# Optimization experiments

Measured on AMD Instinct MI355X. Metric: run time of the kernel, lower is better.

## Reference

```python
import jax, jax.numpy as jnp
import numpy as np

DIM = 512
NUM_ITEM = 2048
K = 10


def setup_inputs() -> dict:
    key = jax.random.key(0)
    k1, k2, k3 = jax.random.split(key, 3)
    input1 = jax.random.normal(k1, (16, DIM, 32, 32), dtype=jnp.float32)
    input2 = jax.random.normal(k2, (16, DIM, 32, 32), dtype=jnp.float32)
    stdv = 1.0 / np.sqrt(DIM)
    mempool = jax.random.uniform(k3, (NUM_ITEM, DIM), minval=-stdv, maxval=stdv, dtype=jnp.float32)
    return {"input1": input1, "input2": input2, "mempool": mempool}


def _memorize(x, mempool):
    # x: [B, C, H, W] with C == DIM
    B, C, H, W = x.shape
    q = jnp.transpose(x, (0, 2, 3, 1)).reshape(-1, C)      # [N, C]
    att = jax.nn.softmax(q @ mempool.T, axis=1)            # [N, num_item]
    val, idx = jax.lax.top_k(att, K)                       # [N, K]
    val = jax.nn.softmax(val, axis=1)                      # renormalize top-k
    # scatter(val into zeros) @ mempool == gather rows of mempool and combine
    out = jnp.einsum('nk,nkd->nd', val, mempool[idx])      # [N, C]
    return jnp.transpose(out.reshape(B, H, W, C), (0, 3, 1, 2))


def reference(input1, input2, mempool):
    return (_memorize(input1, mempool), _memorize(input2, mempool))
```

## Files before the change

### kernel.cpp

```cpp
#include <hip/hip_runtime.h>
#include <math.h>

typedef __attribute__((ext_vector_type(4))) float f4;
typedef __attribute__((ext_vector_type(8))) _Float16 f16x8;
typedef __attribute__((ext_vector_type(8))) short bf16x8;
typedef __attribute__((ext_vector_type(4))) unsigned short u16x4;
typedef unsigned int u32;
typedef unsigned short u16;

#define DIMC  512
#define NITEM 2048
#define TK    10
#define WSP   (NITEM * DIMC)

#define TPB    512
#define PXB    64
#define RIT    256
#define NRND   8
#define NSLICE 16

#define QB_SZ  12288
#define Q_PL   4096
#define SSTR   66
#define LDS_BYTES 67584
#define MV_F 0
#define MI_F 5120
#define MM_F 10240
#define MS_F 10752
#define WB_F 11264
#define IB_F 11904

#define KSWZ(i) (((i) ^ ((i) >> 2)) & 3)

union h16 { _Float16 h; u16 u; };

__device__ __forceinline__ u32 bf16_rne(float f) {
    u32 u = __float_as_uint(f);
    return (u + 0x7fffu + ((u >> 16) & 1u)) >> 16;
}

__device__ __forceinline__ void split3(float f, u16& ph, u16& pb, u16& pr) {
    h16 a; a.h = (_Float16)f;
    float f0 = (float)a.h;
    ph = a.u;
    pb = (u16)bf16_rne(f);
    pr = (u16)bf16_rne(f - f0);
}

__global__ __launch_bounds__(256)
void preconv_kernel(const float* __restrict__ mp, u16* __restrict__ ws)
{
    int idx = (blockIdx.x * 256 + threadIdx.x) * 4;
    int i  = idx >> 9;
    int k0 = idx & 511;
    f4 v = *(const f4*)(mp + (size_t)i * 512 + k0);
    int s  = k0 >> 5, kl = k0 & 31;
    int lh = (kl >> 2) & 3, pair = kl >> 4;
    u16x4 pH, pB, pR;
#pragma unroll
    for (int e = 0; e < 4; ++e) {
        u16 h, b, r; split3(v[e], h, b, r);
        pH[e] = h; pB[e] = b; pR[e] = r;
    }
    size_t base = (size_t)(i >> 4) * 8192 + (size_t)s * 512
                + (size_t)(lh * 16 + (i & 15)) * 8 + pair * 4;
    *(u16x4*)(ws + 0 * WSP + base) = pH;
    *(u16x4*)(ws + 1 * WSP + base) = pB;
    *(u16x4*)(ws + 2 * WSP + base) = pR;
}

__global__ __launch_bounds__(TPB, 4)
void memorize_mfma(const float* __restrict__ x0, const float* __restrict__ x1,
                   const float* __restrict__ mp, const u16* __restrict__ ws,
                   float* __restrict__ out)
{
    extern __shared__ char ldsb[];
    float* ldsf = (float*)ldsb;

    const int t    = threadIdx.x;
    const int lane = t & 63;
    const int w    = t >> 6;
    const int blk  = blockIdx.x;
    const int img  = blk >> 4;
    const int n0   = (blk & 15) * PXB;
    const int b    = img & 15;

    const float* x  = (img < 16) ? x0 : x1;
    const float* xb = x + (size_t)b * (DIMC * 1024);
    float* ob = out + (img < 16 ? (size_t)0 : (size_t)16 * DIMC * 1024)
                    + (size_t)b * (DIMC * 1024);

    const int l15 = lane & 15;
    const int lh  = lane >> 4;
    const int ksw = lh ^ KSWZ(l15);
    const int ig  = w >> 1;
    const int pg  = w & 1;

    const int qp = t & 63;
    const int g  = t >> 6;

    float tv[TK]; int tix[TK];
#pragma unroll
    for (int q = 0; q < TK; ++q) { tv[q] = -INFINITY; tix[q] = 0x7fffffff; }
    float rm = -INFINITY, rs = 0.0f;

    const int scl  = t & 31;
    const int spx  = (t >> 5) << 2;
    const int spos = (((scl >> 2) & 3) << 3) + ((scl >> 4) << 2) + (scl & 3);
    const int sslot = spos >> 3;
    const int soff  = (spos & 7) << 1;

    const u16* aw = ws + (size_t)lane * 8 + (size_t)(ig * 4) * 8192;

    const int qfb = (pg << 11) + (l15 << 6) + (ksw << 4);

#define STAGE_Q(S, BUF)                                                        \
    {                                                                          \
        const float* src = xb + (size_t)(((S) << 5) + scl) * 1024 + n0 + spx;  \
        f4 v = *(const f4*)src;                                                \
        _Pragma("unroll")                                                      \
        for (int e = 0; e < 4; ++e) {                                          \
            int px = spx + e;                                                  \
            u16 h, bb, rr; split3(v[e], h, bb, rr);                            \
            int ro = (BUF) * QB_SZ + (px << 6)                                 \
                   + (((sslot ^ KSWZ(px)) << 4) | soff);                       \
            *(u16*)(ldsb + ro)            = h;                                 \
            *(u16*)(ldsb + ro + Q_PL)     = bb;                                \
            *(u16*)(ldsb + ro + 2 * Q_PL) = rr;                                \
        }                                                                      \
    }

#define ALOAD(IT, S)                                                           \
    {                                                                          \
        const u16* ap = ar + ((size_t)(IT) << 13) + ((S) << 9);                \
        aH[IT] = *(const f16x8*) (ap + 0 * WSP);                               \
        aB[IT] = *(const bf16x8*)(ap + 1 * WSP);                               \
        aR[IT] = *(const bf16x8*)(ap + 2 * WSP);                               \
    }

#pragma unroll 1
    for (int r = 0; r < NRND; ++r) {
        const u16* ar = aw + ((size_t)r << 17);
        f4 acc[4][2];
#pragma unroll
        for (int it = 0; it < 4; ++it)
#pragma unroll
            for (int pt = 0; pt < 2; ++pt) acc[it][pt] = (f4){0.f, 0.f, 0.f, 0.f};

        __syncthreads();
        STAGE_Q(0, 0)
        __syncthreads();

#pragma unroll 1
        for (int s = 0; s < NSLICE; ++s) {
            const int cur = s & 1;

            f16x8 aH[4]; bf16x8 aB[4], aR[4];
            ALOAD(0, s)
            ALOAD(1, s)

            if (s + 1 < NSLICE) STAGE_Q(s + 1, cur ^ 1)

            const char* qc = ldsb + cur * QB_SZ + qfb;
            f16x8 qH[2]; bf16x8 qB[2], qR[2];
#pragma unroll
            for (int pt = 0; pt < 2; ++pt) {
                qH[pt] = *(const f16x8*) (qc + 0 * Q_PL + pt * 1024);
                qB[pt] = *(const bf16x8*)(qc + 1 * Q_PL + pt * 1024);
                qR[pt] = *(const bf16x8*)(qc + 2 * Q_PL + pt * 1024);
            }

#pragma unroll
            for (int it = 0; it < 4; ++it) {
                if (it < 2) ALOAD(it + 2, s)
#pragma unroll
                for (int pt = 0; pt < 2; ++pt) {
                    f4 c = acc[it][pt];
                    c = __builtin_amdgcn_mfma_f32_16x16x32_f16 (aH[it], qH[pt], c, 0, 0, 0);
                    c = __builtin_amdgcn_mfma_f32_16x16x32_bf16(aB[it], qR[pt], c, 0, 0, 0);
                    c = __builtin_amdgcn_mfma_f32_16x16x32_bf16(aR[it], qB[pt], c, 0, 0, 0);
                    acc[it][pt] = c;
                }
            }
            __syncthreads();
        }

#pragma unroll
        for (int it = 0; it < 4; ++it) {
#pragma unroll
            for (int pt = 0; pt < 2; ++pt) {
                int row = (ig << 6) + (it << 4) + (lh << 2);
                int col = (pg << 5) + (pt << 4) + l15;
                float* sp = ldsf + row * SSTR + col;
                sp[0 * SSTR] = acc[it][pt][0];
                sp[1 * SSTR] = acc[it][pt][1];
                sp[2 * SSTR] = acc[it][pt][2];
                sp[3 * SSTR] = acc[it][pt][3];
            }
        }
        __syncthreads();

        float mloc = rm;
#pragma unroll 4
        for (int jj = 0; jj < 32; ++jj) {
            int   il = (g << 5) + jj;
            float v  = ldsf[il * SSTR + qp];
            mloc = fmaxf(mloc, v);
            if (v > tv[TK - 1]) {
                int   id = r * RIT + il;
                float cv = v; int ci = id;
#pragma unroll
                for (int q = 0; q < TK; ++q) {
                    bool  gt = cv > tv[q];
                    float nv = gt ? tv[q]  : cv;
                    int   ni = gt ? tix[q] : ci;
                    tv[q]  = gt ? cv : tv[q];
                    tix[q] = gt ? ci : tix[q];
                    cv = nv; ci = ni;
                }
            }
        }
        rs *= __expf(rm - mloc);
        rm = mloc;
#pragma unroll 4
        for (int jj = 0; jj < 32; ++jj) {
            int   il = (g << 5) + jj;
            float v  = ldsf[il * SSTR + qp];
            rs += __expf(v - rm);
        }
    }

    __syncthreads();
    {
#pragma unroll
        for (int q = 0; q < TK; ++q) {
            ldsf[MV_F + (qp * 8 + g) * TK + q] = tv[q];
            ldsf[MI_F + (qp * 8 + g) * TK + q] = __int_as_float(tix[q]);
        }
        ldsf[MM_F + qp * 8 + g] = rm;
        ldsf[MS_F + qp * 8 + g] = rs;
    }
    __syncthreads();

    if (t < 64) {
        const int p = t;
        float gm[8], gs[8];
#pragma unroll
        for (int G = 0; G < 8; ++G) {
            gm[G] = ldsf[MM_F + p * 8 + G];
            gs[G] = ldsf[MS_F + p * 8 + G];
        }
        float mstar = gm[0];
#pragma unroll
        for (int G = 1; G < 8; ++G) mstar = fmaxf(mstar, gm[G]);
        float Z = 0.0f;
#pragma unroll
        for (int G = 0; G < 8; ++G) Z += gs[G] * __expf(gm[G] - mstar);

        int h0=0,h1=0,h2=0,h3=0,h4=0,h5=0,h6=0,h7=0;
        float ov[TK]; int oi[TK];
#pragma unroll
        for (int o = 0; o < TK; ++o) {
            float bv = -INFINITY; int bi = 0x7fffffff; int bg = 0;
#define SEL(G, HG)                                                               \
            {                                                                    \
                float v  = ldsf[MV_F + (p * 8 + G) * TK + (HG)];                 \
                int   id = __float_as_int(ldsf[MI_F + (p * 8 + G) * TK + (HG)]); \
                if (v > bv || (v == bv && id < bi)) { bv = v; bi = id; bg = G; } \
            }
            SEL(0, h0) SEL(1, h1) SEL(2, h2) SEL(3, h3)
            SEL(4, h4) SEL(5, h5) SEL(6, h6) SEL(7, h7)
#undef SEL
            ov[o] = bv; oi[o] = bi;
            h0 += (bg == 0); h1 += (bg == 1); h2 += (bg == 2); h3 += (bg == 3);
            h4 += (bg == 4); h5 += (bg == 5); h6 += (bg == 6); h7 += (bg == 7);
        }
        float pv[TK];
#pragma unroll
        for (int o = 0; o < TK; ++o) pv[o] = __expf(ov[o] - mstar) / Z;
        float pmax = pv[0];
        float wgt[TK]; float W = 0.0f;
#pragma unroll
        for (int o = 0; o < TK; ++o) { wgt[o] = __expf(pv[o] - pmax); W += wgt[o]; }
#pragma unroll
        for (int o = 0; o < TK; ++o) {
            ldsf[WB_F + p * TK + o] = wgt[o] / W;
            ldsf[IB_F + p * TK + o] = __int_as_float(oi[o]);
        }
    }
    __syncthreads();

    {
        const int ep = t & 63, cg = t >> 6;
        float wr[TK]; const float* rows[TK];
#pragma unroll
        for (int o = 0; o < TK; ++o) {
            wr[o]   = ldsf[WB_F + ep * TK + o];
            rows[o] = mp + (size_t)__float_as_int(ldsf[IB_F + ep * TK + o]) * DIMC;
        }
        float* obase = ob + n0 + ep;
#pragma unroll 4
        for (int cc = 0; cc < 16; ++cc) {
            int c = cg * 64 + cc * 4;
            f4 a = {0.0f, 0.0f, 0.0f, 0.0f};
#pragma unroll
            for (int o = 0; o < TK; ++o) {
                f4 rv = *(const f4*)(rows[o] + c);
#pragma unroll
                for (int z = 0; z < 4; ++z) a[z] = fmaf(wr[o], rv[z], a[z]);
            }
#pragma unroll
            for (int z = 0; z < 4; ++z) obase[(size_t)(c + z) * 1024] = a[z];
        }
    }
#undef STAGE_Q
#undef ALOAD
}

extern "C" void kernel_launch(void* const* d_in, const int* in_sizes, int n_in,
                              void* d_out, int out_size, void* d_ws, size_t ws_size,
                              hipStream_t stream) {
    const float* x0  = (const float*)d_in[0];
    const float* x1  = (const float*)d_in[1];
    const float* mpl = (const float*)d_in[2];
    float* out = (float*)d_out;
    u16* ws = (u16*)d_ws;

    preconv_kernel<<<dim3(1024), dim3(256), 0, stream>>>(mpl, ws);
    memorize_mfma<<<dim3(512), dim3(TPB), LDS_BYTES, stream>>>(x0, x1, mpl, ws, out);
}
```

Measured before the change: 579.5 us.

## Pre-split inputs into MFMA fragment layout in workspace, load directly from global

Adds a preconversion kernel that splits both inputs into fp16/bf16/residual planes laid out in MFMA fragment order inside the workspace. The main kernel then reads the query fragments straight from global memory instead of staging them through double-buffered LDS, which removes the per-slice barriers and the in-loop conversion. This costs an extra pass that writes about 200MB of workspace and reads it back, and depends on the workspace being large enough; otherwise the old LDS-staged path is used.

```diff
diff --git a/kernel.cpp b/kernel.cpp
--- a/kernel.cpp
+++ b/kernel.cpp
@@ -12,6 +12,8 @@
 #define NITEM 2048
 #define TK    10
 #define WSP   (NITEM * DIMC)
+#define XWSP  (32 * DIMC * 1024)
+#define QWS_OFF (3 * WSP)
 
 #define TPB    512
 #define PXB    64
@@ -19,10 +21,7 @@
 #define NRND   8
 #define NSLICE 16
 
-#define QB_SZ  12288
-#define Q_PL   4096
 #define SSTR   66
-#define LDS_BYTES 67584
 #define MV_F 0
 #define MI_F 5120
 #define MM_F 10240
@@ -30,6 +29,9 @@
 #define WB_F 11264
 #define IB_F 11904
 
+#define QB_SZ  12288
+#define Q_PL   4096
+#define LDS_BYTES 67584
 #define KSWZ(i) (((i) ^ ((i) >> 2)) & 3)
 
 union h16 { _Float16 h; u16 u; };
@@ -69,10 +71,244 @@
     *(u16x4*)(ws + 2 * WSP + base) = pR;
 }
 
+__global__ __launch_bounds__(256)
+void preconv_x_kernel(const float* __restrict__ x0, const float* __restrict__ x1,
+                      u16* __restrict__ ws)
+{
+    int T   = blockIdx.x * 256 + threadIdx.x;
+    int px  = T & 1023;
+    int c4  = (T >> 10) & 127;
+    int img = T >> 17;
+    const float* x = (img < 16) ? x0 : x1;
+    const float* src = x + ((size_t)(img & 15) * 512 + (size_t)c4 * 4) * 1024 + px;
+    int s = c4 >> 3, pair = (c4 >> 2) & 1, lh = c4 & 3;
+    u16x4 pH, pB, pR;
+#pragma unroll
+    for (int j = 0; j < 4; ++j) {
+        u16 h, b, r; split3(src[(size_t)j * 1024], h, b, r);
+        pH[j] = h; pB[j] = b; pR[j] = r;
+    }
+    size_t base = (size_t)QWS_OFF
+                + (size_t)(img * 64 + (px >> 4)) * 8192 + (size_t)s * 512
+                + (size_t)((lh * 16 + (px & 15)) << 3) + pair * 4;
+    *(u16x4*)(ws + base + 0 * (size_t)XWSP) = pH;
+    *(u16x4*)(ws + base + 1 * (size_t)XWSP) = pB;
+    *(u16x4*)(ws + base + 2 * (size_t)XWSP) = pR;
+}
+
 __global__ __launch_bounds__(TPB, 4)
-void memorize_mfma(const float* __restrict__ x0, const float* __restrict__ x1,
-                   const float* __restrict__ mp, const u16* __restrict__ ws,
-                   float* __restrict__ out)
+void memorize_direct(const float* __restrict__ mp, const u16* __restrict__ ws,
+                     float* __restrict__ out)
+{
+    __shared__ float ldsf[16896];
+
+    const int t    = threadIdx.x;
+    const int lane = t & 63;
+    const int w    = t >> 6;
+    const int blk  = blockIdx.x;
+    const int img  = blk >> 4;
+    const int n0   = (blk & 15) * PXB;
+
+    float* ob = out + (img < 16 ? (size_t)0 : (size_t)16 * DIMC * 1024)
+                    + (size_t)(img & 15) * (DIMC * 1024);
+
+    const int l15 = lane & 15;
+    const int lh  = lane >> 4;
+    const int ig  = w >> 1;
+    const int pg  = w & 1;
+
+    const int qp = t & 63;
+    const int g  = t >> 6;
+
+    float tv[TK]; int tix[TK];
+#pragma unroll
+    for (int q = 0; q < TK; ++q) { tv[q] = -INFINITY; tix[q] = 0x7fffffff; }
+    float rm = -INFINITY, rs = 0.0f;
+
+    const u16* aw = ws + (size_t)lane * 8 + (size_t)(ig * 4) * 8192;
+    const int G0 = img * 64 + (blk & 15) * 4 + pg * 2;
+    const u16* bw = ws + (size_t)QWS_OFF + (size_t)G0 * 8192 + (size_t)lane * 8;
+
+#define ALOAD(IT, S)                                                           \
+    {                                                                          \
+        const u16* ap = ar + ((size_t)(IT) << 13) + ((S) << 9);                \
+        aH[IT] = *(const f16x8*) (ap + 0 * WSP);                               \
+        aB[IT] = *(const bf16x8*)(ap + 1 * WSP);                               \
+        aR[IT] = *(const bf16x8*)(ap + 2 * WSP);                               \
+    }
+
+#pragma unroll 1
+    for (int r = 0; r < NRND; ++r) {
+        const u16* ar = aw + ((size_t)r << 17);
+        f4 acc[4][2];
+#pragma unroll
+        for (int it = 0; it < 4; ++it)
+#pragma unroll
+            for (int pt = 0; pt < 2; ++pt) acc[it][pt] = (f4){0.f, 0.f, 0.f, 0.f};
+
+#pragma unroll 1
+        for (int s = 0; s < NSLICE; ++s) {
+            f16x8 qH[2]; bf16x8 qB[2], qR[2];
+#pragma unroll
+            for (int pt = 0; pt < 2; ++pt) {
+                const u16* bp = bw + ((size_t)pt << 13) + ((size_t)s << 9);
+                qH[pt] = *(const f16x8*) (bp + 0 * (size_t)XWSP);
+                qB[pt] = *(const bf16x8*)(bp + 1 * (size_t)XWSP);
+                qR[pt] = *(const bf16x8*)(bp + 2 * (size_t)XWSP);
+            }
+            f16x8 aH[4]; bf16x8 aB[4], aR[4];
+            ALOAD(0, s)
+            ALOAD(1, s)
+#pragma unroll
+            for (int it = 0; it < 4; ++it) {
+                if (it < 2) ALOAD(it + 2, s)
+#pragma unroll
+                for (int pt = 0; pt < 2; ++pt) {
+                    f4 c = acc[it][pt];
+                    c = __builtin_amdgcn_mfma_f32_16x16x32_f16 (aH[it], qH[pt], c, 0, 0, 0);
+                    c = __builtin_amdgcn_mfma_f32_16x16x32_bf16(aB[it], qR[pt], c, 0, 0, 0);
+                    c = __builtin_amdgcn_mfma_f32_16x16x32_bf16(aR[it], qB[pt], c, 0, 0, 0);
+                    acc[it][pt] = c;
+                }
+            }
+        }
+
+        __syncthreads();
+#pragma unroll
+        for (int it = 0; it < 4; ++it) {
+#pragma unroll
+            for (int pt = 0; pt < 2; ++pt) {
+                int row = (ig << 6) + (it << 4) + (lh << 2);
+                int col = (pg << 5) + (pt << 4) + l15;
+                float* sp = ldsf + row * SSTR + col;
+                sp[0 * SSTR] = acc[it][pt][0];
+                sp[1 * SSTR] = acc[it][pt][1];
+                sp[2 * SSTR] = acc[it][pt][2];
+                sp[3 * SSTR] = acc[it][pt][3];
+            }
+        }
+        __syncthreads();
+
+        float mloc = rm;
+#pragma unroll 4
+        for (int jj = 0; jj < 32; ++jj) {
+            int   il = (g << 5) + jj;
+            float v  = ldsf[il * SSTR + qp];
+            mloc = fmaxf(mloc, v);
+            if (v > tv[TK - 1]) {
+                int   id = r * RIT + il;
+                float cv = v; int ci = id;
+#pragma unroll
+                for (int q = 0; q < TK; ++q) {
+                    bool  gt = cv > tv[q];
+                    float nv = gt ? tv[q]  : cv;
+                    int   ni = gt ? tix[q] : ci;
+                    tv[q]  = gt ? cv : tv[q];
+                    tix[q] = gt ? ci : tix[q];
+                    cv = nv; ci = ni;
+                }
+            }
+        }
+        rs *= __expf(rm - mloc);
+        rm = mloc;
+#pragma unroll 4
+        for (int jj = 0; jj < 32; ++jj) {
+            int   il = (g << 5) + jj;
+            float v  = ldsf[il * SSTR + qp];
+            rs += __expf(v - rm);
+        }
+    }
+#undef ALOAD
+
+    __syncthreads();
+    {
+#pragma unroll
+        for (int q = 0; q < TK; ++q) {
+            ldsf[MV_F + (qp * 8 + g) * TK + q] = tv[q];
+            ldsf[MI_F + (qp * 8 + g) * TK + q] = __int_as_float(tix[q]);
+        }
+        ldsf[MM_F + qp * 8 + g] = rm;
+        ldsf[MS_F + qp * 8 + g] = rs;
+    }
+    __syncthreads();
+
+    if (t < 64) {
+        const int p = t;
+        float gm[8], gs[8];
+#pragma unroll
+        for (int G = 0; G < 8; ++G) {
+            gm[G] = ldsf[MM_F + p * 8 + G];
+            gs[G] = ldsf[MS_F + p * 8 + G];
+        }
+        float mstar = gm[0];
+#pragma unroll
+        for (int G = 1; G < 8; ++G) mstar = fmaxf(mstar, gm[G]);
+        float Z = 0.0f;
+#pragma unroll
+        for (int G = 0; G < 8; ++G) Z += gs[G] * __expf(gm[G] - mstar);
+
+        int h0=0,h1=0,h2=0,h3=0,h4=0,h5=0,h6=0,h7=0;
+        float ov[TK]; int oi[TK];
+#pragma unroll
+        for (int o = 0; o < TK; ++o) {
+            float bv = -INFINITY; int bi = 0x7fffffff; int bg = 0;
+#define SEL(G, HG)                                                               \
+            {                                                                    \
+                float v  = ldsf[MV_F + (p * 8 + G) * TK + (HG)];                 \
+                int   id = __float_as_int(ldsf[MI_F + (p * 8 + G) * TK + (HG)]); \
+                if (v > bv || (v == bv && id < bi)) { bv = v; bi = id; bg = G; } \
+            }
+            SEL(0, h0) SEL(1, h1) SEL(2, h2) SEL(3, h3)
+            SEL(4, h4) SEL(5, h5) SEL(6, h6) SEL(7, h7)
+#undef SEL
+            ov[o] = bv; oi[o] = bi;
+            h0 += (bg == 0); h1 += (bg == 1); h2 += (bg == 2); h3 += (bg == 3);
+            h4 += (bg == 4); h5 += (bg == 5); h6 += (bg == 6); h7 += (bg == 7);
+        }
+        float pv[TK];
+#pragma unroll
+        for (int o = 0; o < TK; ++o) pv[o] = __expf(ov[o] - mstar) / Z;
+        float pmax = pv[0];
+        float wgt[TK]; float W = 0.0f;
+#pragma unroll
+        for (int o = 0; o < TK; ++o) { wgt[o] = __expf(pv[o] - pmax); W += wgt[o]; }
+#pragma unroll
+        for (int o = 0; o < TK; ++o) {
+            ldsf[WB_F + p * TK + o] = wgt[o] / W;
+            ldsf[IB_F + p * TK + o] = __int_as_float(oi[o]);
+        }
+    }
+    __syncthreads();
+
+    {
+        const int ep = t & 63, cg = t >> 6;
+        float wr[TK]; const float* rows[TK];
+#pragma unroll
+        for (int o = 0; o < TK; ++o) {
+            wr[o]   = ldsf[WB_F + ep * TK + o];
+            rows[o] = mp + (size_t)__float_as_int(ldsf[IB_F + ep * TK + o]) * DIMC;
+        }
+        float* obase = ob + n0 + ep;
+#pragma unroll 4
+        for (int cc = 0; cc < 16; ++cc) {
+            int c = cg * 64 + cc * 4;
+            f4 a = {0.0f, 0.0f, 0.0f, 0.0f};
+#pragma unroll
+            for (int o = 0; o < TK; ++o) {
+                f4 rv = *(const f4*)(rows[o] + c);
+#pragma unroll
+                for (int z = 0; z < 4; ++z) a[z] = fmaf(wr[o], rv[z], a[z]);
+            }
+#pragma unroll
+            for (int z = 0; z < 4; ++z) obase[(size_t)(c + z) * 1024] = a[z];
+        }
+    }
+}
+
+__global__ __launch_bounds__(TPB, 4)
+void memorize_fb(const float* __restrict__ x0, const float* __restrict__ x1,
+                 const float* __restrict__ mp, const u16* __restrict__ ws,
+                 float* __restrict__ out)
 {
     extern __shared__ char ldsb[];
     float* ldsf = (float*)ldsb;
@@ -95,7 +331,6 @@
     const int ksw = lh ^ KSWZ(l15);
     const int ig  = w >> 1;
     const int pg  = w & 1;
-
     const int qp = t & 63;
     const int g  = t >> 6;
 
@@ -111,7 +346,6 @@
     const int soff  = (spos & 7) << 1;
 
     const u16* aw = ws + (size_t)lane * 8 + (size_t)(ig * 4) * 8192;
-
     const int qfb = (pg << 11) + (l15 << 6) + (ksw << 4);
 
 #define STAGE_Q(S, BUF)                                                        \
@@ -130,7 +364,7 @@
         }                                                                      \
     }
 
-#define ALOAD(IT, S)                                                           \
+#define ALOADF(IT, S)                                                          \
     {                                                                          \
         const u16* ap = ar + ((size_t)(IT) << 13) + ((S) << 9);                \
         aH[IT] = *(const f16x8*) (ap + 0 * WSP);                               \
@@ -154,11 +388,9 @@
 #pragma unroll 1
         for (int s = 0; s < NSLICE; ++s) {
             const int cur = s & 1;
-
             f16x8 aH[4]; bf16x8 aB[4], aR[4];
-            ALOAD(0, s)
-            ALOAD(1, s)
-
+            ALOADF(0, s)
+            ALOADF(1, s)
             if (s + 1 < NSLICE) STAGE_Q(s + 1, cur ^ 1)
 
             const char* qc = ldsb + cur * QB_SZ + qfb;
@@ -169,10 +401,9 @@
                 qB[pt] = *(const bf16x8*)(qc + 1 * Q_PL + pt * 1024);
                 qR[pt] = *(const bf16x8*)(qc + 2 * Q_PL + pt * 1024);
             }
-
 #pragma unroll
             for (int it = 0; it < 4; ++it) {
-                if (it < 2) ALOAD(it + 2, s)
+                if (it < 2) ALOADF(it + 2, s)
 #pragma unroll
                 for (int pt = 0; pt < 2; ++pt) {
                     f4 c = acc[it][pt];
@@ -229,6 +460,8 @@
             rs += __expf(v - rm);
         }
     }
+#undef STAGE_Q
+#undef ALOADF
 
     __syncthreads();
     {
@@ -313,8 +546,6 @@
             for (int z = 0; z < 4; ++z) obase[(size_t)(c + z) * 1024] = a[z];
         }
     }
-#undef STAGE_Q
-#undef ALOAD
 }
 
 extern "C" void kernel_launch(void* const* d_in, const int* in_sizes, int n_in,
@@ -326,6 +557,13 @@
     float* out = (float*)d_out;
     u16* ws = (u16*)d_ws;
 
+    const size_t ws_need = ((size_t)QWS_OFF + 3ull * (size_t)XWSP) * 2ull;
+
     preconv_kernel<<<dim3(1024), dim3(256), 0, stream>>>(mpl, ws);
-    memorize_mfma<<<dim3(512), dim3(TPB), LDS_BYTES, stream>>>(x0, x1, mpl, ws, out);
-}
+    if (ws_size >= ws_need) {
+        preconv_x_kernel<<<dim3(16384), dim3(256), 0, stream>>>(x0, x1, ws);
+        memorize_direct<<<dim3(512), dim3(TPB), 0, stream>>>(mpl, ws, out);
+    } else {
+        memorize_fb<<<dim3(512), dim3(TPB), LDS_BYTES, stream>>>(x0, x1, mpl, ws, out);
+    }
+}
```

New measurement: 590.0 us. Within noise of the previous version (+1.8%).
